# Optimization experiments

Hardware: AMD Instinct MI355X
Metric: run time of the kernel (lower is better)

Reference implementation:

```python
import jax, jax.numpy as jnp
import numpy as np

B, S, D = 2, 2048, 512
E, H, TOP_K = 8, 1024, 2
SCALE = 1.0


def setup_inputs() -> dict:
    key = jax.random.key(0)
    ks = jax.random.split(key, 7)
    s = lambda fan_in: 1.0 / np.sqrt(fan_in)
    return {
        "x": jax.random.normal(ks[0], (B, S, D), dtype=jnp.float32),
        "gate_w": jax.random.normal(ks[1], (E, D), dtype=jnp.float32) * s(D),
        "w1": jax.random.normal(ks[2], (E, H, D), dtype=jnp.float32) * s(D),
        "w2": jax.random.normal(ks[3], (E, D, H), dtype=jnp.float32) * s(H),
        "sg_gate": jax.random.normal(ks[4], (H, D), dtype=jnp.float32) * s(D),
        "sg_up": jax.random.normal(ks[5], (H, D), dtype=jnp.float32) * s(D),
        "sg_down": jax.random.normal(ks[6], (D, H), dtype=jnp.float32) * s(H),
    }


def reference(x, gate_w, w1, w2, sg_gate, sg_up, sg_down):
    b, s_len, d = x.shape
    xf = x.reshape(-1, d)                      # [N, D]
    n = xf.shape[0]

    # --- TopKRouter: logits -> top-k -> softmax over the k selected logits ---
    logits = (xf @ gate_w.T) * SCALE           # [N, E]
    topk_w, idx = jax.lax.top_k(logits, TOP_K)  # [N, K]
    topk_w = jax.nn.softmax(topk_w, axis=-1)
    # per-token combine weights scattered to expert slots: [N, E]
    comb = jnp.zeros((n, E), dtype=xf.dtype).at[jnp.arange(n)[:, None], idx].add(topk_w)

    # --- Routed experts (dense masked compute; weight 0 for unrouted) ---
    h = jax.nn.silu(jnp.einsum('td,ehd->teh', xf, w1))   # [N, E, H]
    eo = jnp.einsum('teh,edh->ted', h, w2)               # [N, E, D]
    routed = jnp.einsum('te,ted->td', comb, eo)          # [N, D]

    # --- Shared expert (SwiGLU), n_shared_experts = 1 ---
    shared = (jax.nn.silu(xf @ sg_gate.T) * (xf @ sg_up.T)) @ sg_down.T

    return (routed + shared).reshape(b, s_len, d)
```

## Files before the change

kernel.cpp:

```cpp
#include <hip/hip_runtime.h>
#include <hip/hip_bf16.h>


#define NTOK 4096
#define DDIM 512
#define HDIM 1024
#define NEXP 8
#define CAP  4096

typedef unsigned short u16;
typedef __attribute__((ext_vector_type(8))) short short8;
typedef __attribute__((ext_vector_type(4))) float f32x4;

__device__ __forceinline__ u16 f2bf(float f) {
  unsigned u = __float_as_uint(f);
  u += 0x7fffu + ((u >> 16) & 1u);
  return (u16)(u >> 16);
}
__device__ __forceinline__ float bf2f(u16 v) {
  return __uint_as_float(((unsigned)v) << 16);
}
__device__ __forceinline__ float silu_f(float v) { return v / (1.0f + __expf(-v)); }

__device__ __forceinline__ void gload16(const u16* g, u16* l) {
  __builtin_amdgcn_global_load_lds((const __attribute__((address_space(1))) void*)g,
                                   (__attribute__((address_space(3))) void*)l, 16, 0, 0);
}

__global__ __launch_bounds__(256) void prep(
    const float* __restrict__ x,   const float* __restrict__ gw,
    const float* __restrict__ w1,  const float* __restrict__ w2,
    const float* __restrict__ sgg, const float* __restrict__ sgu,
    const float* __restrict__ sgd,
    u16* __restrict__ Xb, u16* __restrict__ W1b, u16* __restrict__ W2b,
    u16* __restrict__ SGGb, u16* __restrict__ SGUb, u16* __restrict__ SGDb,
    int* __restrict__ tIdx, float2* __restrict__ tW) {
  if (blockIdx.x < NTOK / 4) {
    const int lane = threadIdx.x & 63;
    const int wid  = threadIdx.x >> 6;
    const int t = blockIdx.x * 4 + wid;
    const float4* xr = (const float4*)(x + (size_t)t * DDIM + lane * 8);
    const float4 x0 = xr[0], x1 = xr[1];
    short8 xbv;
    xbv[0]=f2bf(x0.x); xbv[1]=f2bf(x0.y); xbv[2]=f2bf(x0.z); xbv[3]=f2bf(x0.w);
    xbv[4]=f2bf(x1.x); xbv[5]=f2bf(x1.y); xbv[6]=f2bf(x1.z); xbv[7]=f2bf(x1.w);
    *(short8*)&Xb[(size_t)t * DDIM + lane * 8] = xbv;
    float p[NEXP];
#pragma unroll
    for (int e = 0; e < NEXP; ++e) {
      const float4* gr = (const float4*)(gw + (size_t)e * DDIM + lane * 8);
      const float4 g0 = gr[0], g1 = gr[1];
      p[e] = x0.x*g0.x + x0.y*g0.y + x0.z*g0.z + x0.w*g0.w +
             x1.x*g1.x + x1.y*g1.y + x1.z*g1.z + x1.w*g1.w;
    }
#pragma unroll
    for (int e = 0; e < NEXP; ++e) {
#pragma unroll
      for (int m = 32; m >= 1; m >>= 1) p[e] += __shfl_xor(p[e], m);
    }
    if (lane == 0) {
      int i0 = 0; float v0 = p[0];
#pragma unroll
      for (int e = 1; e < NEXP; ++e) if (p[e] > v0) { v0 = p[e]; i0 = e; }
      int i1 = -1; float v1 = -3.0e38f;
#pragma unroll
      for (int e = 0; e < NEXP; ++e) if (e != i0 && p[e] > v1) { v1 = p[e]; i1 = e; }
      const float ex1 = __expf(v1 - v0);
      const float inv = 1.0f / (1.0f + ex1);
      tIdx[t] = i0 | (i1 << 4);
      tW[t] = make_float2(inv, ex1 * inv);
    }
  } else {
    constexpr int NW1 = NEXP * HDIM * DDIM / 4;
    constexpr int NSG = HDIM * DDIM / 4;
    constexpr int TOT = 2 * NW1 + 3 * NSG;
    int i = (blockIdx.x - NTOK / 4) * 256 + threadIdx.x;
    const int stride = (gridDim.x - NTOK / 4) * 256;
    for (; i < TOT; i += stride) {
      const float* s; u16* d; int j = i;
      if (j < NW1)               { s = w1;  d = W1b;  }
      else if ((j -= NW1) < NW1) { s = w2;  d = W2b;  }
      else if ((j -= NW1) < NSG) { s = sgg; d = SGGb; }
      else if ((j -= NSG) < NSG) { s = sgu; d = SGUb; }
      else        { j -= NSG;      s = sgd; d = SGDb; }
      float4 v = ((const float4*)s)[j];
      ushort4 o;
      o.x = f2bf(v.x); o.y = f2bf(v.y); o.z = f2bf(v.z); o.w = f2bf(v.w);
      ((ushort4*)d)[j] = o;
    }
  }
}

__global__ __launch_bounds__(256) void build_lists(
    const int* __restrict__ tIdx,
    int* __restrict__ counts, int* __restrict__ elist) {
  const int e = blockIdx.x;
  __shared__ int cnt;
  if (threadIdx.x == 0) cnt = 0;
  __syncthreads();
  const int lane = threadIdx.x & 63;
  int* el = elist + e * CAP;
  for (int base = 0; base < NTOK; base += 256) {
    const int t = base + threadIdx.x;
    const int pk = tIdx[t];
#pragma unroll
    for (int slot = 0; slot < 2; ++slot) {
      const bool m = (((pk >> (slot * 4)) & 15) == e);
      const unsigned long long b = __ballot(m);
      const int my  = __popcll(b & ((1ull << lane) - 1));
      const int tot = __popcll(b);
      int wbase = 0;
      if (lane == 0 && tot) wbase = atomicAdd(&cnt, tot);
      wbase = __shfl(wbase, 0);
      if (m) el[wbase + my] = t * 2 + slot;
    }
  }
  __syncthreads();
  if (threadIdx.x == 0) counts[e] = cnt;
}

#define BUFE (128 * 32)

__global__ __launch_bounds__(256, 3) void gemm_up(
    const u16* __restrict__ Xb, const u16* __restrict__ W1b,
    const u16* __restrict__ SGGb, const u16* __restrict__ SGUb,
    u16* __restrict__ Hbuf, u16* __restrict__ Gtmp, u16* __restrict__ Utmp,
    const int* __restrict__ counts, const int* __restrict__ elist) {
  constexpr int KDIM = DDIM, KSTEP = KDIM / 32;
  const int z = blockIdx.z;
  const int n0 = blockIdx.x * 128;
  const int m0 = blockIdx.y * 128;
  const bool routed = (z < NEXP);

  int mlim; const u16* Bp; const int* lst = nullptr;
  if (routed) {
    mlim = counts[z];
    lst = elist + z * CAP;
    Bp = W1b + (size_t)z * HDIM * KDIM;
  } else {
    mlim = NTOK;
    Bp = (z == NEXP) ? SGGb : SGUb;
  }
  if (m0 >= mlim) return;

  __shared__ __align__(16) u16 As[3 * BUFE];
  __shared__ __align__(16) u16 Bs[3 * BUFE];
  __shared__ int rowE[128];

  const int tid = threadIdx.x;
  const int wid = tid >> 6, lane = tid & 63;

  if (routed) {
    if (tid < 128) {
      int idx = m0 + tid; if (idx > mlim - 1) idx = mlim - 1;
      rowE[tid] = lst[idx];
    }
    __syncthreads();
  }

  const int sl0 = ((wid)     * 64 + lane) * 8;
  const int sl1 = ((wid + 4) * 64 + lane) * 8;
  const int r0 = (sl0 / 8) >> 2, kc0 = (sl0 / 8) & 3;
  const int r1 = (sl1 / 8) >> 2, kc1 = (sl1 / 8) & 3;
  const int ar0 = routed ? (rowE[r0] >> 1) : (m0 + r0);
  const int ar1 = routed ? (rowE[r1] >> 1) : (m0 + r1);
  const u16* aG0 = Xb + (size_t)ar0 * KDIM + kc0 * 8;
  const u16* aG1 = Xb + (size_t)ar1 * KDIM + kc1 * 8;
  const u16* bG0 = Bp + (size_t)(n0 + r0) * KDIM + kc0 * 8;
  const u16* bG1 = Bp + (size_t)(n0 + r1) * KDIM + kc1 * 8;

  const int wm = (wid >> 1) * 64, wn = (wid & 1) * 64;
  const int lr = lane & 15, lk = lane >> 4;

  const f32x4 zero = {0.f, 0.f, 0.f, 0.f};
  f32x4 acc[4][4];
#pragma unroll
  for (int i = 0; i < 4; ++i)
#pragma unroll
    for (int j = 0; j < 4; ++j) acc[i][j] = zero;

  auto STAGE = [&](int kt, int c) {
    u16* a = As + c * BUFE; u16* b = Bs + c * BUFE;
    gload16(aG0 + kt * 32, a + sl0);
    gload16(aG1 + kt * 32, a + sl1);
    gload16(bG0 + kt * 32, b + sl0);
    gload16(bG1 + kt * 32, b + sl1);
  };

  STAGE(0, 0); STAGE(1, 1);
  int cur = 0;
  for (int kt = 0; kt < KSTEP; ++kt) {
    if (kt + 1 < KSTEP) asm volatile("s_waitcnt vmcnt(4)" ::: "memory");
    else                asm volatile("s_waitcnt vmcnt(0)" ::: "memory");
    __builtin_amdgcn_s_barrier();
    if (kt + 2 < KSTEP) STAGE(kt + 2, cur == 0 ? 2 : cur - 1);
    const u16* ab = As + cur * BUFE;
    const u16* bb = Bs + cur * BUFE;
    short8 a[4], b[4];
#pragma unroll
    for (int i = 0; i < 4; ++i)
      a[i] = *(const short8*)&ab[(wm + i * 16 + lr) * 32 + lk * 8];
#pragma unroll
    for (int j = 0; j < 4; ++j)
      b[j] = *(const short8*)&bb[(wn + j * 16 + lr) * 32 + lk * 8];
    asm volatile("s_waitcnt lgkmcnt(0)" ::: "memory");
    __builtin_amdgcn_sched_barrier(0);
#pragma unroll
    for (int i = 0; i < 4; ++i)
#pragma unroll
      for (int j = 0; j < 4; ++j)
        acc[i][j] = __builtin_amdgcn_mfma_f32_16x16x32_bf16(a[i], b[j], acc[i][j], 0, 0, 0);
    cur = (cur == 2) ? 0 : cur + 1;
  }

#pragma unroll
  for (int i = 0; i < 4; ++i) {
#pragma unroll
    for (int j = 0; j < 4; ++j) {
      const int col = n0 + wn + j * 16 + lr;
#pragma unroll
      for (int r = 0; r < 4; ++r) {
        const int m = wm + i * 16 + lk * 4 + r;
        if (routed) {
          if (m0 + m < mlim)
            Hbuf[(size_t)rowE[m] * HDIM + col] = f2bf(silu_f(acc[i][j][r]));
        } else if (z == NEXP) {
          Gtmp[(size_t)(m0 + m) * HDIM + col] = f2bf(silu_f(acc[i][j][r]));
        } else {
          Utmp[(size_t)(m0 + m) * HDIM + col] = f2bf(acc[i][j][r]);
        }
      }
    }
  }
}

__global__ __launch_bounds__(256) void fuse_act(
    const u16* __restrict__ G, const u16* __restrict__ U, u16* __restrict__ ACT) {
  const int i = blockIdx.x * 256 + threadIdx.x;
  const short8 g = *(const short8*)&G[(size_t)i * 8];
  const short8 u = *(const short8*)&U[(size_t)i * 8];
  short8 o;
#pragma unroll
  for (int k = 0; k < 8; ++k)
    o[k] = (short)f2bf(bf2f((u16)g[k]) * bf2f((u16)u[k]));
  *(short8*)&ACT[(size_t)i * 8] = o;
}

__global__ __launch_bounds__(256, 3) void gemm_down(
    const u16* __restrict__ Hbuf, const u16* __restrict__ W2b,
    const u16* __restrict__ ACT,  const u16* __restrict__ SGDb,
    u16* __restrict__ eo0, u16* __restrict__ eo1,
    float* __restrict__ sh0, float* __restrict__ sh1,
    const int* __restrict__ counts, const int* __restrict__ elist) {
  constexpr int KFULL = HDIM;
  constexpr int KSTEP = 512 / 32;
  const int z = blockIdx.z;
  const int n0 = blockIdx.x * 128;
  const int m0 = blockIdx.y * 128;
  const bool routed = (z < 2 * NEXP);
  const int khalf = routed ? (z & 1) : (z - 2 * NEXP);
  const int koff = khalf * 512;

  int mlim; const u16* Ap; const u16* Bp; const int* lst = nullptr;
  if (routed) {
    const int e = z >> 1;
    mlim = counts[e];
    lst = elist + e * CAP;
    Ap = Hbuf;
    Bp = W2b + (size_t)e * DDIM * KFULL;
  } else {
    mlim = NTOK;
    Ap = ACT;
    Bp = SGDb;
  }
  if (m0 >= mlim) return;

  __shared__ __align__(16) u16 As[3 * BUFE];
  __shared__ __align__(16) u16 Bs[3 * BUFE];
  __shared__ int rowE[128];

  const int tid = threadIdx.x;
  const int wid = tid >> 6, lane = tid & 63;

  if (routed) {
    if (tid < 128) {
      int idx = m0 + tid; if (idx > mlim - 1) idx = mlim - 1;
      rowE[tid] = lst[idx];
    }
    __syncthreads();
  }

  const int sl0 = ((wid)     * 64 + lane) * 8;
  const int sl1 = ((wid + 4) * 64 + lane) * 8;
  const int r0 = (sl0 / 8) >> 2, kc0 = (sl0 / 8) & 3;
  const int r1 = (sl1 / 8) >> 2, kc1 = (sl1 / 8) & 3;
  const int ar0 = routed ? rowE[r0] : (m0 + r0);
  const int ar1 = routed ? rowE[r1] : (m0 + r1);
  const u16* aG0 = Ap + (size_t)ar0 * KFULL + koff + kc0 * 8;
  const u16* aG1 = Ap + (size_t)ar1 * KFULL + koff + kc1 * 8;
  const u16* bG0 = Bp + (size_t)(n0 + r0) * KFULL + koff + kc0 * 8;
  const u16* bG1 = Bp + (size_t)(n0 + r1) * KFULL + koff + kc1 * 8;

  const int wm = (wid >> 1) * 64, wn = (wid & 1) * 64;
  const int lr = lane & 15, lk = lane >> 4;

  const f32x4 zero = {0.f, 0.f, 0.f, 0.f};
  f32x4 acc[4][4];
#pragma unroll
  for (int i = 0; i < 4; ++i)
#pragma unroll
    for (int j = 0; j < 4; ++j) acc[i][j] = zero;

  auto STAGE = [&](int kt, int c) {
    u16* a = As + c * BUFE; u16* b = Bs + c * BUFE;
    gload16(aG0 + kt * 32, a + sl0);
    gload16(aG1 + kt * 32, a + sl1);
    gload16(bG0 + kt * 32, b + sl0);
    gload16(bG1 + kt * 32, b + sl1);
  };

  STAGE(0, 0); STAGE(1, 1);
  int cur = 0;
  for (int kt = 0; kt < KSTEP; ++kt) {
    if (kt + 1 < KSTEP) asm volatile("s_waitcnt vmcnt(4)" ::: "memory");
    else                asm volatile("s_waitcnt vmcnt(0)" ::: "memory");
    __builtin_amdgcn_s_barrier();
    if (kt + 2 < KSTEP) STAGE(kt + 2, cur == 0 ? 2 : cur - 1);
    const u16* ab = As + cur * BUFE;
    const u16* bb = Bs + cur * BUFE;
    short8 a[4], b[4];
#pragma unroll
    for (int i = 0; i < 4; ++i)
      a[i] = *(const short8*)&ab[(wm + i * 16 + lr) * 32 + lk * 8];
#pragma unroll
    for (int j = 0; j < 4; ++j)
      b[j] = *(const short8*)&bb[(wn + j * 16 + lr) * 32 + lk * 8];
    asm volatile("s_waitcnt lgkmcnt(0)" ::: "memory");
    __builtin_amdgcn_sched_barrier(0);
#pragma unroll
    for (int i = 0; i < 4; ++i)
#pragma unroll
      for (int j = 0; j < 4; ++j)
        acc[i][j] = __builtin_amdgcn_mfma_f32_16x16x32_bf16(a[i], b[j], acc[i][j], 0, 0, 0);
    cur = (cur == 2) ? 0 : cur + 1;
  }

#pragma unroll
  for (int i = 0; i < 4; ++i) {
#pragma unroll
    for (int j = 0; j < 4; ++j) {
      const int col = n0 + wn + j * 16 + lr;
#pragma unroll
      for (int r = 0; r < 4; ++r) {
        const int m = wm + i * 16 + lk * 4 + r;
        if (routed) {
          if (m0 + m < mlim) {
            u16* dst = khalf ? eo1 : eo0;
            dst[(size_t)rowE[m] * DDIM + col] = f2bf(acc[i][j][r]);
          }
        } else {
          float* dst = khalf ? sh1 : sh0;
          dst[(size_t)(m0 + m) * DDIM + col] = acc[i][j][r];
        }
      }
    }
  }
}

__global__ __launch_bounds__(256) void combine_kernel(
    const u16* __restrict__ eo0, const u16* __restrict__ eo1,
    const float* __restrict__ sh0, const float* __restrict__ sh1,
    const float2* __restrict__ tW, float* __restrict__ out) {
  const int g = blockIdx.x * 256 + threadIdx.x;
  const int t = g >> 6;
  const int c0 = (g & 63) * 8;
  const float2 w = tW[t];
  const size_t r0 = (size_t)(t * 2) * DDIM + c0;
  const size_t r1 = (size_t)(t * 2 + 1) * DDIM + c0;
  const short8 a0 = *(const short8*)&eo0[r0];
  const short8 a1 = *(const short8*)&eo0[r1];
  const short8 b0 = *(const short8*)&eo1[r0];
  const short8 b1 = *(const short8*)&eo1[r1];
  const size_t so = (size_t)t * DDIM + c0;
  const float4 s0a = ((const float4*)(sh0 + so))[0];
  const float4 s0b = ((const float4*)(sh0 + so))[1];
  const float4 s1a = ((const float4*)(sh1 + so))[0];
  const float4 s1b = ((const float4*)(sh1 + so))[1];
  float o[8];
  o[0]=s0a.x+s1a.x; o[1]=s0a.y+s1a.y; o[2]=s0a.z+s1a.z; o[3]=s0a.w+s1a.w;
  o[4]=s0b.x+s1b.x; o[5]=s0b.y+s1b.y; o[6]=s0b.z+s1b.z; o[7]=s0b.w+s1b.w;
#pragma unroll
  for (int k = 0; k < 8; ++k)
    o[k] += w.x * (bf2f((u16)a0[k]) + bf2f((u16)b0[k])) +
            w.y * (bf2f((u16)a1[k]) + bf2f((u16)b1[k]));
  float4 v0 = {o[0], o[1], o[2], o[3]};
  float4 v1 = {o[4], o[5], o[6], o[7]};
  ((float4*)(out + so))[0] = v0;
  ((float4*)(out + so))[1] = v1;
}

extern "C" void kernel_launch(void* const* d_in, const int* in_sizes, int n_in,
                              void* d_out, int out_size, void* d_ws, size_t ws_size,
                              hipStream_t stream) {
  const float* x    = (const float*)d_in[0];
  const float* gw   = (const float*)d_in[1];
  const float* w1   = (const float*)d_in[2];
  const float* w2   = (const float*)d_in[3];
  const float* sgg  = (const float*)d_in[4];
  const float* sgu  = (const float*)d_in[5];
  const float* sgd  = (const float*)d_in[6];
  float* out = (float*)d_out;

  char* ws = (char*)d_ws;
  size_t off = 0;
  auto take = [&](size_t bytes) {
    size_t r = off; off += (bytes + 255) & ~(size_t)255; return r;
  };
  int*    counts = (int*)   (ws + take(NEXP * sizeof(int)));
  int*    elist  = (int*)   (ws + take((size_t)NEXP * CAP * sizeof(int)));
  int*    tIdx   = (int*)   (ws + take((size_t)NTOK * sizeof(int)));
  float2* tW     = (float2*)(ws + take((size_t)NTOK * sizeof(float2)));
  u16*    Xb     = (u16*)   (ws + take((size_t)NTOK * DDIM * 2));
  u16*    W1b    = (u16*)   (ws + take((size_t)NEXP * HDIM * DDIM * 2));
  u16*    W2b    = (u16*)   (ws + take((size_t)NEXP * DDIM * HDIM * 2));
  u16*    SGGb   = (u16*)   (ws + take((size_t)HDIM * DDIM * 2));
  u16*    SGUb   = (u16*)   (ws + take((size_t)HDIM * DDIM * 2));
  u16*    SGDb   = (u16*)   (ws + take((size_t)DDIM * HDIM * 2));
  u16*    Hbuf   = (u16*)   (ws + take((size_t)NTOK * 2 * HDIM * 2));
  u16*    ACT    = (u16*)   (ws + take((size_t)NTOK * HDIM * 2));
  u16*    Gtmp   = (u16*)   (ws + take((size_t)NTOK * HDIM * 2));
  u16*    Utmp   = (u16*)   (ws + take((size_t)NTOK * HDIM * 2));
  u16*    eo0    = (u16*)   (ws + take((size_t)NTOK * 2 * DDIM * 2));
  u16*    eo1    = (u16*)   (ws + take((size_t)NTOK * 2 * DDIM * 2));
  float*  sh0    = (float*) (ws + take((size_t)NTOK * DDIM * 4));
  float*  sh1    = (float*) (ws + take((size_t)NTOK * DDIM * 4));
  if (off > ws_size) return;

  prep<<<dim3(3072), 256, 0, stream>>>(x, gw, w1, w2, sgg, sgu, sgd,
                                       Xb, W1b, W2b, SGGb, SGUb, SGDb, tIdx, tW);
  build_lists<<<NEXP, 256, 0, stream>>>(tIdx, counts, elist);
  gemm_up<<<dim3(HDIM / 128, 32, NEXP + 2), 256, 0, stream>>>(
      Xb, W1b, SGGb, SGUb, Hbuf, Gtmp, Utmp, counts, elist);
  fuse_act<<<NTOK * HDIM / 8 / 256, 256, 0, stream>>>(Gtmp, Utmp, ACT);
  gemm_down<<<dim3(DDIM / 128, 32, 2 * NEXP + 2), 256, 0, stream>>>(
      Hbuf, W2b, ACT, SGDb, eo0, eo1, sh0, sh1, counts, elist);
  combine_kernel<<<NTOK * 64 / 256, 256, 0, stream>>>(eo0, eo1, sh0, sh1, tW, out);
}
```

Baseline: 115.3 us.

## Deepen GEMM prefetch pipeline to four LDS stages and swizzle LDS layout

Both expert GEMM kernels go from a 3-buffer to a 4-buffer LDS ring, prefetching three K-steps ahead with adjusted vmcnt waits. Shared-memory tiles now use an XOR-style rotation of the 16-byte K chunks per row pair, applied on the global-to-LDS store and the MFMA operand reads, to cut LDS bank conflicts. The larger LDS footprint lowers the occupancy hint from 3 to 2 blocks per CU, trading latency-hiding parallelism for deeper per-block prefetch.

```diff
diff --git a/kernel.cpp b/kernel.cpp
--- a/kernel.cpp
+++ b/kernel.cpp
@@ -121,7 +121,7 @@
 
 #define BUFE (128 * 32)
 
-__global__ __launch_bounds__(256, 3) void gemm_up(
+__global__ __launch_bounds__(256, 2) void gemm_up(
     const u16* __restrict__ Xb, const u16* __restrict__ W1b,
     const u16* __restrict__ SGGb, const u16* __restrict__ SGUb,
     u16* __restrict__ Hbuf, u16* __restrict__ Gtmp, u16* __restrict__ Utmp,
@@ -143,8 +143,8 @@
   }
   if (m0 >= mlim) return;
 
-  __shared__ __align__(16) u16 As[3 * BUFE];
-  __shared__ __align__(16) u16 Bs[3 * BUFE];
+  __shared__ __align__(16) u16 As[4 * BUFE];
+  __shared__ __align__(16) u16 Bs[4 * BUFE];
   __shared__ int rowE[128];
 
   const int tid = threadIdx.x;
@@ -158,19 +158,21 @@
     __syncthreads();
   }
 
-  const int sl0 = ((wid)     * 64 + lane) * 8;
-  const int sl1 = ((wid + 4) * 64 + lane) * 8;
-  const int r0 = (sl0 / 8) >> 2, kc0 = (sl0 / 8) & 3;
-  const int r1 = (sl1 / 8) >> 2, kc1 = (sl1 / 8) & 3;
-  const int ar0 = routed ? (rowE[r0] >> 1) : (m0 + r0);
-  const int ar1 = routed ? (rowE[r1] >> 1) : (m0 + r1);
-  const u16* aG0 = Xb + (size_t)ar0 * KDIM + kc0 * 8;
-  const u16* aG1 = Xb + (size_t)ar1 * KDIM + kc1 * 8;
-  const u16* bG0 = Bp + (size_t)(n0 + r0) * KDIM + kc0 * 8;
-  const u16* bG1 = Bp + (size_t)(n0 + r1) * KDIM + kc1 * 8;
+  const int sidx0 = wid * 64 + lane;
+  const int sidx1 = (wid + 4) * 64 + lane;
+  const int row0 = sidx0 >> 2, row1 = sidx1 >> 2;
+  const int kcp0 = ((sidx0 & 3) - ((row0 >> 1) & 3)) & 3;
+  const int kcp1 = ((sidx1 & 3) - ((row1 >> 1) & 3)) & 3;
+  const int ar0 = routed ? (rowE[row0] >> 1) : (m0 + row0);
+  const int ar1 = routed ? (rowE[row1] >> 1) : (m0 + row1);
+  const u16* aG0 = Xb + (size_t)ar0 * KDIM + kcp0 * 8;
+  const u16* aG1 = Xb + (size_t)ar1 * KDIM + kcp1 * 8;
+  const u16* bG0 = Bp + (size_t)(n0 + row0) * KDIM + kcp0 * 8;
+  const u16* bG1 = Bp + (size_t)(n0 + row1) * KDIM + kcp1 * 8;
 
   const int wm = (wid >> 1) * 64, wn = (wid & 1) * 64;
   const int lr = lane & 15, lk = lane >> 4;
+  const int rslot = ((lk + ((lr >> 1) & 3)) & 3) * 8;
 
   const f32x4 zero = {0.f, 0.f, 0.f, 0.f};
   f32x4 acc[4][4];
@@ -181,28 +183,28 @@
 
   auto STAGE = [&](int kt, int c) {
     u16* a = As + c * BUFE; u16* b = Bs + c * BUFE;
-    gload16(aG0 + kt * 32, a + sl0);
-    gload16(aG1 + kt * 32, a + sl1);
-    gload16(bG0 + kt * 32, b + sl0);
-    gload16(bG1 + kt * 32, b + sl1);
+    gload16(aG0 + kt * 32, a + sidx0 * 8);
+    gload16(aG1 + kt * 32, a + sidx1 * 8);
+    gload16(bG0 + kt * 32, b + sidx0 * 8);
+    gload16(bG1 + kt * 32, b + sidx1 * 8);
   };
 
-  STAGE(0, 0); STAGE(1, 1);
-  int cur = 0;
+  STAGE(0, 0); STAGE(1, 1); STAGE(2, 2);
   for (int kt = 0; kt < KSTEP; ++kt) {
-    if (kt + 1 < KSTEP) asm volatile("s_waitcnt vmcnt(4)" ::: "memory");
-    else                asm volatile("s_waitcnt vmcnt(0)" ::: "memory");
+    if (kt + 2 < KSTEP)      asm volatile("s_waitcnt vmcnt(8)" ::: "memory");
+    else if (kt + 1 < KSTEP) asm volatile("s_waitcnt vmcnt(4)" ::: "memory");
+    else                     asm volatile("s_waitcnt vmcnt(0)" ::: "memory");
     __builtin_amdgcn_s_barrier();
-    if (kt + 2 < KSTEP) STAGE(kt + 2, cur == 0 ? 2 : cur - 1);
-    const u16* ab = As + cur * BUFE;
-    const u16* bb = Bs + cur * BUFE;
+    if (kt + 3 < KSTEP) STAGE(kt + 3, (kt + 3) & 3);
+    const u16* ab = As + (kt & 3) * BUFE;
+    const u16* bb = Bs + (kt & 3) * BUFE;
     short8 a[4], b[4];
 #pragma unroll
     for (int i = 0; i < 4; ++i)
-      a[i] = *(const short8*)&ab[(wm + i * 16 + lr) * 32 + lk * 8];
+      a[i] = *(const short8*)&ab[(wm + i * 16 + lr) * 32 + rslot];
 #pragma unroll
     for (int j = 0; j < 4; ++j)
-      b[j] = *(const short8*)&bb[(wn + j * 16 + lr) * 32 + lk * 8];
+      b[j] = *(const short8*)&bb[(wn + j * 16 + lr) * 32 + rslot];
     asm volatile("s_waitcnt lgkmcnt(0)" ::: "memory");
     __builtin_amdgcn_sched_barrier(0);
 #pragma unroll
@@ -210,7 +212,6 @@
 #pragma unroll
       for (int j = 0; j < 4; ++j)
         acc[i][j] = __builtin_amdgcn_mfma_f32_16x16x32_bf16(a[i], b[j], acc[i][j], 0, 0, 0);
-    cur = (cur == 2) ? 0 : cur + 1;
   }
 
 #pragma unroll
@@ -246,7 +247,7 @@
   *(short8*)&ACT[(size_t)i * 8] = o;
 }
 
-__global__ __launch_bounds__(256, 3) void gemm_down(
+__global__ __launch_bounds__(256, 2) void gemm_down(
     const u16* __restrict__ Hbuf, const u16* __restrict__ W2b,
     const u16* __restrict__ ACT,  const u16* __restrict__ SGDb,
     u16* __restrict__ eo0, u16* __restrict__ eo1,
@@ -275,8 +276,8 @@
   }
   if (m0 >= mlim) return;
 
-  __shared__ __align__(16) u16 As[3 * BUFE];
-  __shared__ __align__(16) u16 Bs[3 * BUFE];
+  __shared__ __align__(16) u16 As[4 * BUFE];
+  __shared__ __align__(16) u16 Bs[4 * BUFE];
   __shared__ int rowE[128];
 
   const int tid = threadIdx.x;
@@ -290,19 +291,21 @@
     __syncthreads();
   }
 
-  const int sl0 = ((wid)     * 64 + lane) * 8;
-  const int sl1 = ((wid + 4) * 64 + lane) * 8;
-  const int r0 = (sl0 / 8) >> 2, kc0 = (sl0 / 8) & 3;
-  const int r1 = (sl1 / 8) >> 2, kc1 = (sl1 / 8) & 3;
-  const int ar0 = routed ? rowE[r0] : (m0 + r0);
-  const int ar1 = routed ? rowE[r1] : (m0 + r1);
-  const u16* aG0 = Ap + (size_t)ar0 * KFULL + koff + kc0 * 8;
-  const u16* aG1 = Ap + (size_t)ar1 * KFULL + koff + kc1 * 8;
-  const u16* bG0 = Bp + (size_t)(n0 + r0) * KFULL + koff + kc0 * 8;
-  const u16* bG1 = Bp + (size_t)(n0 + r1) * KFULL + koff + kc1 * 8;
+  const int sidx0 = wid * 64 + lane;
+  const int sidx1 = (wid + 4) * 64 + lane;
+  const int row0 = sidx0 >> 2, row1 = sidx1 >> 2;
+  const int kcp0 = ((sidx0 & 3) - ((row0 >> 1) & 3)) & 3;
+  const int kcp1 = ((sidx1 & 3) - ((row1 >> 1) & 3)) & 3;
+  const int ar0 = routed ? rowE[row0] : (m0 + row0);
+  const int ar1 = routed ? rowE[row1] : (m0 + row1);
+  const u16* aG0 = Ap + (size_t)ar0 * KFULL + koff + kcp0 * 8;
+  const u16* aG1 = Ap + (size_t)ar1 * KFULL + koff + kcp1 * 8;
+  const u16* bG0 = Bp + (size_t)(n0 + row0) * KFULL + koff + kcp0 * 8;
+  const u16* bG1 = Bp + (size_t)(n0 + row1) * KFULL + koff + kcp1 * 8;
 
   const int wm = (wid >> 1) * 64, wn = (wid & 1) * 64;
   const int lr = lane & 15, lk = lane >> 4;
+  const int rslot = ((lk + ((lr >> 1) & 3)) & 3) * 8;
 
   const f32x4 zero = {0.f, 0.f, 0.f, 0.f};
   f32x4 acc[4][4];
@@ -313,28 +316,28 @@
 
   auto STAGE = [&](int kt, int c) {
     u16* a = As + c * BUFE; u16* b = Bs + c * BUFE;
-    gload16(aG0 + kt * 32, a + sl0);
-    gload16(aG1 + kt * 32, a + sl1);
-    gload16(bG0 + kt * 32, b + sl0);
-    gload16(bG1 + kt * 32, b + sl1);
+    gload16(aG0 + kt * 32, a + sidx0 * 8);
+    gload16(aG1 + kt * 32, a + sidx1 * 8);
+    gload16(bG0 + kt * 32, b + sidx0 * 8);
+    gload16(bG1 + kt * 32, b + sidx1 * 8);
   };
 
-  STAGE(0, 0); STAGE(1, 1);
-  int cur = 0;
+  STAGE(0, 0); STAGE(1, 1); STAGE(2, 2);
   for (int kt = 0; kt < KSTEP; ++kt) {
-    if (kt + 1 < KSTEP) asm volatile("s_waitcnt vmcnt(4)" ::: "memory");
-    else                asm volatile("s_waitcnt vmcnt(0)" ::: "memory");
+    if (kt + 2 < KSTEP)      asm volatile("s_waitcnt vmcnt(8)" ::: "memory");
+    else if (kt + 1 < KSTEP) asm volatile("s_waitcnt vmcnt(4)" ::: "memory");
+    else                     asm volatile("s_waitcnt vmcnt(0)" ::: "memory");
     __builtin_amdgcn_s_barrier();
-    if (kt + 2 < KSTEP) STAGE(kt + 2, cur == 0 ? 2 : cur - 1);
-    const u16* ab = As + cur * BUFE;
-    const u16* bb = Bs + cur * BUFE;
+    if (kt + 3 < KSTEP) STAGE(kt + 3, (kt + 3) & 3);
+    const u16* ab = As + (kt & 3) * BUFE;
+    const u16* bb = Bs + (kt & 3) * BUFE;
     short8 a[4], b[4];
 #pragma unroll
     for (int i = 0; i < 4; ++i)
-      a[i] = *(const short8*)&ab[(wm + i * 16 + lr) * 32 + lk * 8];
+      a[i] = *(const short8*)&ab[(wm + i * 16 + lr) * 32 + rslot];
 #pragma unroll
     for (int j = 0; j < 4; ++j)
-      b[j] = *(const short8*)&bb[(wn + j * 16 + lr) * 32 + lk * 8];
+      b[j] = *(const short8*)&bb[(wn + j * 16 + lr) * 32 + rslot];
     asm volatile("s_waitcnt lgkmcnt(0)" ::: "memory");
     __builtin_amdgcn_sched_barrier(0);
 #pragma unroll
@@ -342,7 +345,6 @@
 #pragma unroll
       for (int j = 0; j < 4; ++j)
         acc[i][j] = __builtin_amdgcn_mfma_f32_16x16x32_bf16(a[i], b[j], acc[i][j], 0, 0, 0);
-    cur = (cur == 2) ? 0 : cur + 1;
   }
 
 #pragma unroll
```

Result: slower. 122.6 us (+6.3%).

## Use 512-thread blocks with XOR-style swizzled LDS layout in expert GEMMs

Applied to the files above, without the earlier changes.

Both expert GEMM kernels move from 256 to 512 threads per block. Each of the 8 waves now computes a 64x32 sub-tile instead of 64x64, which halves accumulator registers per wave and raises the occupancy hint. Each thread stages one 16-byte chunk per matrix. The K-chunk placement in LDS is rotated per row pair to reduce bank conflicts on the MFMA fragment reads. The cost is more waves sharing each barrier and lower per-wave reuse of A fragments, since each wave issues 8 MFMAs per K step instead of 16.

```diff
diff --git a/kernel.cpp b/kernel.cpp
--- a/kernel.cpp
+++ b/kernel.cpp
@@ -121,7 +121,7 @@
 
 #define BUFE (128 * 32)
 
-__global__ __launch_bounds__(256, 3) void gemm_up(
+__global__ __launch_bounds__(512, 6) void gemm_up(
     const u16* __restrict__ Xb, const u16* __restrict__ W1b,
     const u16* __restrict__ SGGb, const u16* __restrict__ SGUb,
     u16* __restrict__ Hbuf, u16* __restrict__ Gtmp, u16* __restrict__ Utmp,
@@ -158,65 +158,56 @@
     __syncthreads();
   }
 
-  const int sl0 = ((wid)     * 64 + lane) * 8;
-  const int sl1 = ((wid + 4) * 64 + lane) * 8;
-  const int r0 = (sl0 / 8) >> 2, kc0 = (sl0 / 8) & 3;
-  const int r1 = (sl1 / 8) >> 2, kc1 = (sl1 / 8) & 3;
-  const int ar0 = routed ? (rowE[r0] >> 1) : (m0 + r0);
-  const int ar1 = routed ? (rowE[r1] >> 1) : (m0 + r1);
-  const u16* aG0 = Xb + (size_t)ar0 * KDIM + kc0 * 8;
-  const u16* aG1 = Xb + (size_t)ar1 * KDIM + kc1 * 8;
-  const u16* bG0 = Bp + (size_t)(n0 + r0) * KDIM + kc0 * 8;
-  const u16* bG1 = Bp + (size_t)(n0 + r1) * KDIM + kc1 * 8;
-
-  const int wm = (wid >> 1) * 64, wn = (wid & 1) * 64;
+  const int row = tid >> 2;
+  const int kcp = ((tid & 3) - ((row >> 1) & 3)) & 3;
+  const int arow = routed ? (rowE[row] >> 1) : (m0 + row);
+  const u16* aG = Xb + (size_t)arow * KDIM + kcp * 8;
+  const u16* bG = Bp + (size_t)(n0 + row) * KDIM + kcp * 8;
+
+  const int wm = (wid >> 2) * 64, wn = (wid & 3) * 32;
   const int lr = lane & 15, lk = lane >> 4;
+  const int rslot = ((lk + ((lr >> 1) & 3)) & 3) * 8;
 
   const f32x4 zero = {0.f, 0.f, 0.f, 0.f};
-  f32x4 acc[4][4];
+  f32x4 acc[4][2];
 #pragma unroll
   for (int i = 0; i < 4; ++i)
 #pragma unroll
-    for (int j = 0; j < 4; ++j) acc[i][j] = zero;
+    for (int j = 0; j < 2; ++j) acc[i][j] = zero;
 
   auto STAGE = [&](int kt, int c) {
-    u16* a = As + c * BUFE; u16* b = Bs + c * BUFE;
-    gload16(aG0 + kt * 32, a + sl0);
-    gload16(aG1 + kt * 32, a + sl1);
-    gload16(bG0 + kt * 32, b + sl0);
-    gload16(bG1 + kt * 32, b + sl1);
+    gload16(aG + kt * 32, As + c * BUFE + tid * 8);
+    gload16(bG + kt * 32, Bs + c * BUFE + tid * 8);
   };
 
   STAGE(0, 0); STAGE(1, 1);
-  int cur = 0;
   for (int kt = 0; kt < KSTEP; ++kt) {
-    if (kt + 1 < KSTEP) asm volatile("s_waitcnt vmcnt(4)" ::: "memory");
+    if (kt + 1 < KSTEP) asm volatile("s_waitcnt vmcnt(2)" ::: "memory");
     else                asm volatile("s_waitcnt vmcnt(0)" ::: "memory");
     __builtin_amdgcn_s_barrier();
-    if (kt + 2 < KSTEP) STAGE(kt + 2, cur == 0 ? 2 : cur - 1);
-    const u16* ab = As + cur * BUFE;
-    const u16* bb = Bs + cur * BUFE;
-    short8 a[4], b[4];
+    if (kt + 2 < KSTEP) STAGE(kt + 2, (kt + 2) % 3);
+    const u16* ab = As + (kt % 3) * BUFE;
+    const u16* bb = Bs + (kt % 3) * BUFE;
+    short8 a[4], b[2];
 #pragma unroll
     for (int i = 0; i < 4; ++i)
-      a[i] = *(const short8*)&ab[(wm + i * 16 + lr) * 32 + lk * 8];
-#pragma unroll
-    for (int j = 0; j < 4; ++j)
-      b[j] = *(const short8*)&bb[(wn + j * 16 + lr) * 32 + lk * 8];
+      a[i] = *(const short8*)&ab[(wm + i * 16 + lr) * 32 + rslot];
+#pragma unroll
+    for (int j = 0; j < 2; ++j)
+      b[j] = *(const short8*)&bb[(wn + j * 16 + lr) * 32 + rslot];
     asm volatile("s_waitcnt lgkmcnt(0)" ::: "memory");
     __builtin_amdgcn_sched_barrier(0);
 #pragma unroll
     for (int i = 0; i < 4; ++i)
 #pragma unroll
-      for (int j = 0; j < 4; ++j)
+      for (int j = 0; j < 2; ++j)
         acc[i][j] = __builtin_amdgcn_mfma_f32_16x16x32_bf16(a[i], b[j], acc[i][j], 0, 0, 0);
-    cur = (cur == 2) ? 0 : cur + 1;
   }
 
 #pragma unroll
   for (int i = 0; i < 4; ++i) {
 #pragma unroll
-    for (int j = 0; j < 4; ++j) {
+    for (int j = 0; j < 2; ++j) {
       const int col = n0 + wn + j * 16 + lr;
 #pragma unroll
       for (int r = 0; r < 4; ++r) {
@@ -246,7 +237,7 @@
   *(short8*)&ACT[(size_t)i * 8] = o;
 }
 
-__global__ __launch_bounds__(256, 3) void gemm_down(
+__global__ __launch_bounds__(512, 6) void gemm_down(
     const u16* __restrict__ Hbuf, const u16* __restrict__ W2b,
     const u16* __restrict__ ACT,  const u16* __restrict__ SGDb,
     u16* __restrict__ eo0, u16* __restrict__ eo1,
@@ -290,65 +281,56 @@
     __syncthreads();
   }
 
-  const int sl0 = ((wid)     * 64 + lane) * 8;
-  const int sl1 = ((wid + 4) * 64 + lane) * 8;
-  const int r0 = (sl0 / 8) >> 2, kc0 = (sl0 / 8) & 3;
-  const int r1 = (sl1 / 8) >> 2, kc1 = (sl1 / 8) & 3;
-  const int ar0 = routed ? rowE[r0] : (m0 + r0);
-  const int ar1 = routed ? rowE[r1] : (m0 + r1);
-  const u16* aG0 = Ap + (size_t)ar0 * KFULL + koff + kc0 * 8;
-  const u16* aG1 = Ap + (size_t)ar1 * KFULL + koff + kc1 * 8;
-  const u16* bG0 = Bp + (size_t)(n0 + r0) * KFULL + koff + kc0 * 8;
-  const u16* bG1 = Bp + (size_t)(n0 + r1) * KFULL + koff + kc1 * 8;
-
-  const int wm = (wid >> 1) * 64, wn = (wid & 1) * 64;
+  const int row = tid >> 2;
+  const int kcp = ((tid & 3) - ((row >> 1) & 3)) & 3;
+  const int arow = routed ? rowE[row] : (m0 + row);
+  const u16* aG = Ap + (size_t)arow * KFULL + koff + kcp * 8;
+  const u16* bG = Bp + (size_t)(n0 + row) * KFULL + koff + kcp * 8;
+
+  const int wm = (wid >> 2) * 64, wn = (wid & 3) * 32;
   const int lr = lane & 15, lk = lane >> 4;
+  const int rslot = ((lk + ((lr >> 1) & 3)) & 3) * 8;
 
   const f32x4 zero = {0.f, 0.f, 0.f, 0.f};
-  f32x4 acc[4][4];
+  f32x4 acc[4][2];
 #pragma unroll
   for (int i = 0; i < 4; ++i)
 #pragma unroll
-    for (int j = 0; j < 4; ++j) acc[i][j] = zero;
+    for (int j = 0; j < 2; ++j) acc[i][j] = zero;
 
   auto STAGE = [&](int kt, int c) {
-    u16* a = As + c * BUFE; u16* b = Bs + c * BUFE;
-    gload16(aG0 + kt * 32, a + sl0);
-    gload16(aG1 + kt * 32, a + sl1);
-    gload16(bG0 + kt * 32, b + sl0);
-    gload16(bG1 + kt * 32, b + sl1);
+    gload16(aG + kt * 32, As + c * BUFE + tid * 8);
+    gload16(bG + kt * 32, Bs + c * BUFE + tid * 8);
   };
 
   STAGE(0, 0); STAGE(1, 1);
-  int cur = 0;
   for (int kt = 0; kt < KSTEP; ++kt) {
-    if (kt + 1 < KSTEP) asm volatile("s_waitcnt vmcnt(4)" ::: "memory");
+    if (kt + 1 < KSTEP) asm volatile("s_waitcnt vmcnt(2)" ::: "memory");
     else                asm volatile("s_waitcnt vmcnt(0)" ::: "memory");
     __builtin_amdgcn_s_barrier();
-    if (kt + 2 < KSTEP) STAGE(kt + 2, cur == 0 ? 2 : cur - 1);
-    const u16* ab = As + cur * BUFE;
-    const u16* bb = Bs + cur * BUFE;
-    short8 a[4], b[4];
+    if (kt + 2 < KSTEP) STAGE(kt + 2, (kt + 2) % 3);
+    const u16* ab = As + (kt % 3) * BUFE;
+    const u16* bb = Bs + (kt % 3) * BUFE;
+    short8 a[4], b[2];
 #pragma unroll
     for (int i = 0; i < 4; ++i)
-      a[i] = *(const short8*)&ab[(wm + i * 16 + lr) * 32 + lk * 8];
-#pragma unroll
-    for (int j = 0; j < 4; ++j)
-      b[j] = *(const short8*)&bb[(wn + j * 16 + lr) * 32 + lk * 8];
+      a[i] = *(const short8*)&ab[(wm + i * 16 + lr) * 32 + rslot];
+#pragma unroll
+    for (int j = 0; j < 2; ++j)
+      b[j] = *(const short8*)&bb[(wn + j * 16 + lr) * 32 + rslot];
     asm volatile("s_waitcnt lgkmcnt(0)" ::: "memory");
     __builtin_amdgcn_sched_barrier(0);
 #pragma unroll
     for (int i = 0; i < 4; ++i)
 #pragma unroll
-      for (int j = 0; j < 4; ++j)
+      for (int j = 0; j < 2; ++j)
         acc[i][j] = __builtin_amdgcn_mfma_f32_16x16x32_bf16(a[i], b[j], acc[i][j], 0, 0, 0);
-    cur = (cur == 2) ? 0 : cur + 1;
   }
 
 #pragma unroll
   for (int i = 0; i < 4; ++i) {
 #pragma unroll
-    for (int j = 0; j < 4; ++j) {
+    for (int j = 0; j < 2; ++j) {
       const int col = n0 + wn + j * 16 + lr;
 #pragma unroll
       for (int r = 0; r < 4; ++r) {
@@ -439,10 +421,10 @@
   prep<<<dim3(3072), 256, 0, stream>>>(x, gw, w1, w2, sgg, sgu, sgd,
                                        Xb, W1b, W2b, SGGb, SGUb, SGDb, tIdx, tW);
   build_lists<<<NEXP, 256, 0, stream>>>(tIdx, counts, elist);
-  gemm_up<<<dim3(HDIM / 128, 32, NEXP + 2), 256, 0, stream>>>(
+  gemm_up<<<dim3(HDIM / 128, 32, NEXP + 2), 512, 0, stream>>>(
       Xb, W1b, SGGb, SGUb, Hbuf, Gtmp, Utmp, counts, elist);
   fuse_act<<<NTOK * HDIM / 8 / 256, 256, 0, stream>>>(Gtmp, Utmp, ACT);
-  gemm_down<<<dim3(DDIM / 128, 32, 2 * NEXP + 2), 256, 0, stream>>>(
+  gemm_down<<<dim3(DDIM / 128, 32, 2 * NEXP + 2), 512, 0, stream>>>(
       Hbuf, W2b, ACT, SGDb, eo0, eo1, sh0, sh1, counts, elist);
   combine_kernel<<<NTOK * 64 / 256, 256, 0, stream>>>(eo0, eo1, sh0, sh1, tW, out);
 }
```

After: 107.5 us. 1.07x faster.
